# Optimization experiments

Hardware: AMD Instinct MI355X
Metric: run time of the kernel (lower is better)

## Reference

```python
import jax, jax.numpy as jnp
import numpy as np

IN_F, HID, OUT, NN = 64, 128, 64, 128
TOTAL = 4096  # 32 graphs * 128 nodes


def setup_inputs() -> dict:
    key = jax.random.key(0)
    ks = jax.random.split(key, 8)
    d_in = 1 + 2 * IN_F
    s1 = 1.0 / np.sqrt(d_in)
    s2 = 1.0 / np.sqrt(HID)
    return {
        "feat": jax.random.normal(ks[0], (TOTAL, IN_F), jnp.float32),
        "coordinate": jax.random.normal(ks[1], (TOTAL, 3), jnp.float32),
        "W1": jax.random.uniform(ks[2], (d_in, HID), jnp.float32, -s1, s1),
        "b1": jax.random.uniform(ks[3], (HID,), jnp.float32, -s1, s1),
        "W2": jax.random.uniform(ks[4], (HID, HID), jnp.float32, -s2, s2),
        "b2": jax.random.uniform(ks[5], (HID,), jnp.float32, -s2, s2),
        "W3": jax.random.uniform(ks[6], (HID, OUT), jnp.float32, -s2, s2),
        "b3": jax.random.uniform(ks[7], (OUT,), jnp.float32, -s2, s2),
        "num_nodes": NN,
    }


def reference(feat, coordinate, W1, b1, W2, b2, W3, b3, num_nodes):
    N = num_nodes
    B = feat.shape[0] // N
    h = feat.reshape(B, N, -1)        # [B,N,F]
    x = coordinate.reshape(B, N, -1)  # [B,N,3]
    # pairwise squared distance: [B,N,N,1]
    d2 = jnp.sum((x[:, None, :, :] - x[:, :, None, :]) ** 2, axis=-1, keepdims=True)
    F = h.shape[-1]
    # feat concat order matches torch: [h_j broadcast over dim1, h_i broadcast over dim2]
    hj = jnp.broadcast_to(h[:, None, :, :], (B, N, N, F))
    hi = jnp.broadcast_to(h[:, :, None, :], (B, N, N, F))
    z = jnp.concatenate([d2, hj, hi], axis=-1)  # [B,N,N,1+2F]
    z = jax.nn.silu(z @ W1 + b1)
    z = jax.nn.silu(z @ W2 + b2)
    z = z @ W3 + b3                   # [B,N,N,OUT]
    return jnp.sum(z, axis=(1, 2))    # [B,OUT]
```

## Files before the change

### kernel.cpp

```cpp
#include <hip/hip_runtime.h>
#include <hip/hip_bf16.h>

#define F_IN 64
#define HID 128
#define OUTF 64
#define NN 128
#define NB 32
#define TOTAL 4096

typedef short bf16x8 __attribute__((ext_vector_type(8)));
typedef float f32x4 __attribute__((ext_vector_type(4)));

static __device__ __forceinline__ short f2bf(float v) {
  __hip_bfloat16 h = __float2bfloat16(v);
  return __builtin_bit_cast(short, h);
}

static __device__ __forceinline__ float fast_silu(float v) {
  return v * __builtin_amdgcn_rcpf(1.f + __expf(-v));
}

__global__ void prep0(const float* __restrict__ feat,
                      const float* __restrict__ W1,
                      const float* __restrict__ W2,
                      __hip_bfloat16* __restrict__ hb,
                      __hip_bfloat16* __restrict__ wcatT,
                      __hip_bfloat16* __restrict__ w2t) {
  int idx = blockIdx.x * 256 + threadIdx.x;
  if (idx < TOTAL * F_IN) hb[idx] = __float2bfloat16(feat[idx]);
  if (idx < 256 * F_IN) {
    int c = idx >> 6, k = idx & 63;
    float wv = (c < HID) ? W1[(1 + k) * HID + c] : W1[(65 + k) * HID + (c - HID)];
    wcatT[idx] = __float2bfloat16(wv);
  }
  if (idx < HID * HID) {
    int c = idx >> 7, k = idx & 127;
    w2t[c * HID + k] = __float2bfloat16(W2[k * HID + c]);
  }
}

__global__ __launch_bounds__(256) void prep_uv(
    const __hip_bfloat16* __restrict__ hb,
    const __hip_bfloat16* __restrict__ wcatT,
    const float* __restrict__ b1,
    float* __restrict__ uv) {
  const int wave = threadIdx.x >> 6, lane = threadIdx.x & 63;
  const int lr = lane & 15, kg = lane >> 4;
  const int r0 = blockIdx.x * 16;
  f32x4 acc[4];
#pragma unroll
  for (int ct = 0; ct < 4; ++ct) acc[ct] = {0.f, 0.f, 0.f, 0.f};
#pragma unroll
  for (int ks = 0; ks < 2; ++ks) {
    bf16x8 a = *reinterpret_cast<const bf16x8*>(hb + (r0 + lr) * F_IN + ks * 32 + kg * 8);
#pragma unroll
    for (int ct = 0; ct < 4; ++ct) {
      const int c = wave * 64 + ct * 16 + lr;
      bf16x8 w = *reinterpret_cast<const bf16x8*>(
          reinterpret_cast<const short*>(wcatT) + c * F_IN + ks * 32 + kg * 8);
      acc[ct] = __builtin_amdgcn_mfma_f32_16x16x32_bf16(a, w, acc[ct], 0, 0, 0);
    }
  }
#pragma unroll
  for (int ct = 0; ct < 4; ++ct) {
    const int c = wave * 64 + ct * 16 + lr;
    const float badd = (c >= HID) ? b1[c - HID] : 0.f;
#pragma unroll
    for (int reg = 0; reg < 4; ++reg) {
      const int r = r0 + kg * 4 + reg;
      uv[(size_t)r * 256 + c] = acc[ct][reg] + badd;
    }
  }
}

__global__ __launch_bounds__(256) void sake_main(
    const float* __restrict__ coord,
    const float* __restrict__ W1,
    const float* __restrict__ b2,
    const float* __restrict__ uv,
    const __hip_bfloat16* __restrict__ w2t,
    float* __restrict__ part) {
  __shared__ __align__(16) char A1[NN * 256];
  __shared__ float d2s[NN];
  __shared__ float ssum[2][HID];

  const int tid = threadIdx.x;
  const int bid = blockIdx.x;
  const int b = bid >> 7;
  const int i = bid & 127;

  if (tid < NN) {
    const float* xj = coord + (size_t)(b * NN + tid) * 3;
    const float* xi = coord + (size_t)(b * NN + i) * 3;
    float dx = xj[0] - xi[0], dy = xj[1] - xi[1], dz = xj[2] - xi[2];
    d2s[tid] = dx * dx + dy * dy + dz * dz;
  }
  __syncthreads();

  {
    const int cg = tid & 15;
    const int rg = tid >> 4;
    const int c0 = cg * 8;
    const f32x4 w0a = *reinterpret_cast<const f32x4*>(W1 + c0);
    const f32x4 w0b = *reinterpret_cast<const f32x4*>(W1 + c0 + 4);
    const float* vbp = uv + (size_t)(b * NN + i) * 256 + HID + c0;
    const f32x4 vba = *reinterpret_cast<const f32x4*>(vbp);
    const f32x4 vbb = *reinterpret_cast<const f32x4*>(vbp + 4);
#pragma unroll
    for (int it = 0; it < 8; ++it) {
      const int r = rg * 8 + it;
      const float* up = uv + (size_t)(b * NN + r) * 256 + c0;
      const f32x4 ua = *reinterpret_cast<const f32x4*>(up);
      const f32x4 ub = *reinterpret_cast<const f32x4*>(up + 4);
      const float d2r = d2s[r];
      bf16x8 pk;
#pragma unroll
      for (int j = 0; j < 4; ++j)
        pk[j] = f2bf(fast_silu(fmaf(d2r, w0a[j], vba[j] + ua[j])));
#pragma unroll
      for (int j = 0; j < 4; ++j)
        pk[4 + j] = f2bf(fast_silu(fmaf(d2r, w0b[j], vbb[j] + ub[j])));
      const int byo = (cg * 16) ^ (it << 4);
      *reinterpret_cast<bf16x8*>(A1 + r * 256 + byo) = pk;
    }
  }
  __syncthreads();

  const int wave = tid >> 6;
  const int lane = tid & 63;
  const int lr = lane & 15;
  const int kg = lane >> 4;
  const int row_off = (wave >> 1) * 64;
  const int col_off = (wave & 1) * 64;

  f32x4 acc[4][4];
#pragma unroll
  for (int ct = 0; ct < 4; ++ct) {
    const float bb = b2[col_off + ct * 16 + lr];
#pragma unroll
    for (int rt = 0; rt < 4; ++rt)
#pragma unroll
      for (int reg = 0; reg < 4; ++reg) acc[rt][ct][reg] = bb;
  }

#pragma unroll
  for (int ks = 0; ks < 4; ++ks) {
    bf16x8 a[4], w[4];
    const int kb = ks * 64 + kg * 16;
#pragma unroll
    for (int rt = 0; rt < 4; ++rt) {
      const int r = row_off + rt * 16 + lr;
      a[rt] = *reinterpret_cast<const bf16x8*>(A1 + r * 256 + (kb ^ ((r & 7) << 4)));
    }
#pragma unroll
    for (int ct = 0; ct < 4; ++ct) {
      const int c = col_off + ct * 16 + lr;
      w[ct] = *reinterpret_cast<const bf16x8*>(
          reinterpret_cast<const short*>(w2t) + c * HID + ks * 32 + kg * 8);
    }
#pragma unroll
    for (int rt = 0; rt < 4; ++rt)
#pragma unroll
      for (int ct = 0; ct < 4; ++ct)
        acc[rt][ct] = __builtin_amdgcn_mfma_f32_16x16x32_bf16(a[rt], w[ct],
                                                              acc[rt][ct], 0, 0, 0);
  }

  float csum[4];
#pragma unroll
  for (int ct = 0; ct < 4; ++ct) {
    float s = 0.f;
#pragma unroll
    for (int rt = 0; rt < 4; ++rt)
#pragma unroll
      for (int reg = 0; reg < 4; ++reg) s += fast_silu(acc[rt][ct][reg]);
    csum[ct] = s;
  }
#pragma unroll
  for (int ct = 0; ct < 4; ++ct) {
    float s = csum[ct];
    s += __shfl_down(s, 32);
    s += __shfl_down(s, 16);
    csum[ct] = s;
  }
  if (lane < 16) {
    const int sel = wave >> 1;
#pragma unroll
    for (int ct = 0; ct < 4; ++ct)
      ssum[sel][col_off + ct * 16 + lane] = csum[ct];
  }
  __syncthreads();
  if (tid < HID)
    part[(size_t)bid * HID + tid] = ssum[0][tid] + ssum[1][tid];
}

__global__ void final_kernel(const float* __restrict__ part,
                             const float* __restrict__ W3,
                             const float* __restrict__ b3,
                             float* __restrict__ out) {
  __shared__ float s2[2][HID];
  __shared__ float s[HID];
  int b = blockIdx.x, t = threadIdx.x;
  int c = t & 127, half = t >> 7;
  float a = 0.f;
  for (int i = half * 64; i < half * 64 + 64; ++i)
    a += part[(size_t)(b * NN + i) * HID + c];
  s2[half][c] = a;
  __syncthreads();
  if (t < HID) s[t] = s2[0][t] + s2[1][t];
  __syncthreads();
  if (t < OUTF) {
    float o = 16384.f * b3[t];
    for (int c2 = 0; c2 < HID; ++c2) o += s[c2] * W3[c2 * OUTF + t];
    out[b * OUTF + t] = o;
  }
}

extern "C" void kernel_launch(void* const* d_in, const int* in_sizes, int n_in,
                              void* d_out, int out_size, void* d_ws, size_t ws_size,
                              hipStream_t stream) {
  const float* feat = (const float*)d_in[0];
  const float* coord = (const float*)d_in[1];
  const float* W1 = (const float*)d_in[2];
  const float* b1 = (const float*)d_in[3];
  const float* W2 = (const float*)d_in[4];
  const float* b2 = (const float*)d_in[5];
  const float* W3 = (const float*)d_in[6];
  const float* b3 = (const float*)d_in[7];
  float* out = (float*)d_out;

  char* ws = (char*)d_ws;
  __hip_bfloat16* hb = (__hip_bfloat16*)ws;
  __hip_bfloat16* wcatT = (__hip_bfloat16*)(ws + 512 * 1024);
  __hip_bfloat16* w2t = (__hip_bfloat16*)(ws + 544 * 1024);
  float* uv = (float*)(ws + 576 * 1024);
  float* part = (float*)(ws + 576 * 1024 + 4096 * 1024);

  prep0<<<1024, 256, 0, stream>>>(feat, W1, W2, hb, wcatT, w2t);
  prep_uv<<<256, 256, 0, stream>>>(hb, wcatT, b1, uv);
  sake_main<<<TOTAL, 256, 0, stream>>>(coord, W1, b2, uv, w2t, part);
  final_kernel<<<NB, 256, 0, stream>>>(part, W3, b3, out);
}
```

Before: 72.87 us.

## Fuse prep kernels, build first-layer activations in registers, stage W2 in LDS

Merges the two prep kernels into one that converts features and W1 on the fly and writes a swizzled bf16 W2. The main kernel now uses 512 threads, with each wave owning 16 j-rows. It computes the silu layer-1 activations directly into MFMA A-fragments instead of staging them through LDS. It also stages W2 in LDS with an XOR swizzle and remaps block IDs to spread graphs across XCDs. This removes one launch and the A1 LDS round trip, at the cost of every block copying 32KB of W2 from global memory and holding more accumulators per wave.

```diff
diff --git a/kernel.cpp b/kernel.cpp
--- a/kernel.cpp
+++ b/kernel.cpp
@@ -15,49 +15,67 @@
   __hip_bfloat16 h = __float2bfloat16(v);
   return __builtin_bit_cast(short, h);
 }
-
 static __device__ __forceinline__ float fast_silu(float v) {
   return v * __builtin_amdgcn_rcpf(1.f + __expf(-v));
 }
 
-__global__ void prep0(const float* __restrict__ feat,
-                      const float* __restrict__ W1,
-                      const float* __restrict__ W2,
-                      __hip_bfloat16* __restrict__ hb,
-                      __hip_bfloat16* __restrict__ wcatT,
-                      __hip_bfloat16* __restrict__ w2t) {
-  int idx = blockIdx.x * 256 + threadIdx.x;
-  if (idx < TOTAL * F_IN) hb[idx] = __float2bfloat16(feat[idx]);
-  if (idx < 256 * F_IN) {
-    int c = idx >> 6, k = idx & 63;
-    float wv = (c < HID) ? W1[(1 + k) * HID + c] : W1[(65 + k) * HID + (c - HID)];
-    wcatT[idx] = __float2bfloat16(wv);
-  }
-  if (idx < HID * HID) {
-    int c = idx >> 7, k = idx & 127;
-    w2t[c * HID + k] = __float2bfloat16(W2[k * HID + c]);
-  }
-}
-
-__global__ __launch_bounds__(256) void prep_uv(
-    const __hip_bfloat16* __restrict__ hb,
-    const __hip_bfloat16* __restrict__ wcatT,
+__global__ __launch_bounds__(256) void uv_prep(
+    const float* __restrict__ feat,
+    const float* __restrict__ W1,
+    const float* __restrict__ W2,
     const float* __restrict__ b1,
-    float* __restrict__ uv) {
-  const int wave = threadIdx.x >> 6, lane = threadIdx.x & 63;
+    float* __restrict__ uv,
+    __hip_bfloat16* __restrict__ w2swz) {
+  __shared__ __align__(16) char wcat[256 * 128];
+  const int tid = threadIdx.x;
+
+  {
+    const int c = tid;
+    const int cc = c & 127;
+    const int rbase = (c < HID) ? 1 : 65;
+#pragma unroll
+    for (int p = 0; p < 8; ++p) {
+      bf16x8 pk;
+#pragma unroll
+      for (int m = 0; m < 8; ++m)
+        pk[m] = f2bf(W1[(rbase + p * 8 + m) * HID + cc]);
+      *reinterpret_cast<bf16x8*>(wcat + c * 128 + ((p ^ (c & 7)) << 4)) = pk;
+    }
+  }
+  if (blockIdx.x < 64) {
+    const int e = blockIdx.x * 256 + tid;
+    const int kk = e >> 7, cc2 = e & 127;
+    const int byo = cc2 * 256 + (((kk >> 3) ^ (cc2 & 7)) << 4) + (kk & 7) * 2;
+    *reinterpret_cast<__hip_bfloat16*>(reinterpret_cast<char*>(w2swz) + byo) =
+        __float2bfloat16(W2[kk * HID + cc2]);
+  }
+  __syncthreads();
+
+  const int wave = tid >> 6, lane = tid & 63;
   const int lr = lane & 15, kg = lane >> 4;
   const int r0 = blockIdx.x * 16;
+
   f32x4 acc[4];
 #pragma unroll
   for (int ct = 0; ct < 4; ++ct) acc[ct] = {0.f, 0.f, 0.f, 0.f};
+
 #pragma unroll
   for (int ks = 0; ks < 2; ++ks) {
-    bf16x8 a = *reinterpret_cast<const bf16x8*>(hb + (r0 + lr) * F_IN + ks * 32 + kg * 8);
+    const float* fp = feat + (size_t)(r0 + lr) * F_IN + ks * 32 + kg * 8;
+    const f32x4 fa = *reinterpret_cast<const f32x4*>(fp);
+    const f32x4 fb = *reinterpret_cast<const f32x4*>(fp + 4);
+    bf16x8 a;
+#pragma unroll
+    for (int m = 0; m < 4; ++m) {
+      a[m] = f2bf(fa[m]);
+      a[4 + m] = f2bf(fb[m]);
+    }
+    const int slot = ks * 4 + kg;
 #pragma unroll
     for (int ct = 0; ct < 4; ++ct) {
       const int c = wave * 64 + ct * 16 + lr;
-      bf16x8 w = *reinterpret_cast<const bf16x8*>(
-          reinterpret_cast<const short*>(wcatT) + c * F_IN + ks * 32 + kg * 8);
+      const bf16x8 w = *reinterpret_cast<const bf16x8*>(
+          wcat + c * 128 + ((slot ^ (c & 7)) << 4));
       acc[ct] = __builtin_amdgcn_mfma_f32_16x16x32_bf16(a, w, acc[ct], 0, 0, 0);
     }
   }
@@ -73,125 +91,93 @@
   }
 }
 
-__global__ __launch_bounds__(256) void sake_main(
+__global__ __launch_bounds__(512) void sake_main(
     const float* __restrict__ coord,
     const float* __restrict__ W1,
     const float* __restrict__ b2,
     const float* __restrict__ uv,
-    const __hip_bfloat16* __restrict__ w2t,
+    const __hip_bfloat16* __restrict__ w2swz,
     float* __restrict__ part) {
-  __shared__ __align__(16) char A1[NN * 256];
-  __shared__ float d2s[NN];
-  __shared__ float ssum[2][HID];
+  __shared__ __align__(16) char w2lds[HID * 256];
+  __shared__ float ssum[8][HID];
 
   const int tid = threadIdx.x;
-  const int bid = blockIdx.x;
+  const int bid = (blockIdx.x & 7) * 512 + (blockIdx.x >> 3);
   const int b = bid >> 7;
   const int i = bid & 127;
 
-  if (tid < NN) {
-    const float* xj = coord + (size_t)(b * NN + tid) * 3;
-    const float* xi = coord + (size_t)(b * NN + i) * 3;
-    float dx = xj[0] - xi[0], dy = xj[1] - xi[1], dz = xj[2] - xi[2];
-    d2s[tid] = dx * dx + dy * dy + dz * dz;
-  }
-  __syncthreads();
-
-  {
-    const int cg = tid & 15;
-    const int rg = tid >> 4;
-    const int c0 = cg * 8;
-    const f32x4 w0a = *reinterpret_cast<const f32x4*>(W1 + c0);
-    const f32x4 w0b = *reinterpret_cast<const f32x4*>(W1 + c0 + 4);
-    const float* vbp = uv + (size_t)(b * NN + i) * 256 + HID + c0;
-    const f32x4 vba = *reinterpret_cast<const f32x4*>(vbp);
-    const f32x4 vbb = *reinterpret_cast<const f32x4*>(vbp + 4);
-#pragma unroll
-    for (int it = 0; it < 8; ++it) {
-      const int r = rg * 8 + it;
-      const float* up = uv + (size_t)(b * NN + r) * 256 + c0;
-      const f32x4 ua = *reinterpret_cast<const f32x4*>(up);
-      const f32x4 ub = *reinterpret_cast<const f32x4*>(up + 4);
-      const float d2r = d2s[r];
-      bf16x8 pk;
-#pragma unroll
-      for (int j = 0; j < 4; ++j)
-        pk[j] = f2bf(fast_silu(fmaf(d2r, w0a[j], vba[j] + ua[j])));
-#pragma unroll
-      for (int j = 0; j < 4; ++j)
-        pk[4 + j] = f2bf(fast_silu(fmaf(d2r, w0b[j], vbb[j] + ub[j])));
-      const int byo = (cg * 16) ^ (it << 4);
-      *reinterpret_cast<bf16x8*>(A1 + r * 256 + byo) = pk;
-    }
-  }
-  __syncthreads();
-
-  const int wave = tid >> 6;
-  const int lane = tid & 63;
-  const int lr = lane & 15;
-  const int kg = lane >> 4;
-  const int row_off = (wave >> 1) * 64;
-  const int col_off = (wave & 1) * 64;
-
-  f32x4 acc[4][4];
-#pragma unroll
-  for (int ct = 0; ct < 4; ++ct) {
-    const float bb = b2[col_off + ct * 16 + lr];
-#pragma unroll
-    for (int rt = 0; rt < 4; ++rt)
-#pragma unroll
-      for (int reg = 0; reg < 4; ++reg) acc[rt][ct][reg] = bb;
-  }
+#pragma unroll
+  for (int p = 0; p < 4; ++p) {
+    const int o = (tid + p * 512) * 16;
+    *reinterpret_cast<int4*>(w2lds + o) =
+        *reinterpret_cast<const int4*>(reinterpret_cast<const char*>(w2swz) + o);
+  }
+
+  const int wave = tid >> 6, lane = tid & 63;
+  const int lr = lane & 15, kg = lane >> 4;
+  const int j = wave * 16 + lr;
+
+  const float* xj = coord + (size_t)(b * NN + j) * 3;
+  const float* xi = coord + (size_t)(b * NN + i) * 3;
+  const float dx = xj[0] - xi[0], dy = xj[1] - xi[1], dz = xj[2] - xi[2];
+  const float d2j = dx * dx + dy * dy + dz * dz;
+
+  f32x4 acc[8];
+#pragma unroll
+  for (int ct = 0; ct < 8; ++ct) {
+    const float bb = b2[ct * 16 + lr];
+    acc[ct] = {bb, bb, bb, bb};
+  }
+
+  const float* urow = uv + (size_t)(b * NN + j) * 256;
+  const float* vrow = uv + (size_t)(b * NN + i) * 256 + HID;
+
+  __syncthreads();
 
 #pragma unroll
   for (int ks = 0; ks < 4; ++ks) {
-    bf16x8 a[4], w[4];
-    const int kb = ks * 64 + kg * 16;
-#pragma unroll
-    for (int rt = 0; rt < 4; ++rt) {
-      const int r = row_off + rt * 16 + lr;
-      a[rt] = *reinterpret_cast<const bf16x8*>(A1 + r * 256 + (kb ^ ((r & 7) << 4)));
-    }
-#pragma unroll
-    for (int ct = 0; ct < 4; ++ct) {
-      const int c = col_off + ct * 16 + lr;
-      w[ct] = *reinterpret_cast<const bf16x8*>(
-          reinterpret_cast<const short*>(w2t) + c * HID + ks * 32 + kg * 8);
-    }
-#pragma unroll
-    for (int rt = 0; rt < 4; ++rt)
-#pragma unroll
-      for (int ct = 0; ct < 4; ++ct)
-        acc[rt][ct] = __builtin_amdgcn_mfma_f32_16x16x32_bf16(a[rt], w[ct],
-                                                              acc[rt][ct], 0, 0, 0);
-  }
-
-  float csum[4];
-#pragma unroll
-  for (int ct = 0; ct < 4; ++ct) {
+    const int c0 = ks * 32 + kg * 8;
+    const f32x4 ua = *reinterpret_cast<const f32x4*>(urow + c0);
+    const f32x4 ub = *reinterpret_cast<const f32x4*>(urow + c0 + 4);
+    const f32x4 va = *reinterpret_cast<const f32x4*>(vrow + c0);
+    const f32x4 vb = *reinterpret_cast<const f32x4*>(vrow + c0 + 4);
+    const f32x4 wa = *reinterpret_cast<const f32x4*>(W1 + c0);
+    const f32x4 wb = *reinterpret_cast<const f32x4*>(W1 + c0 + 4);
+    bf16x8 a;
+#pragma unroll
+    for (int m = 0; m < 4; ++m) {
+      a[m] = f2bf(fast_silu(fmaf(d2j, wa[m], ua[m] + va[m])));
+      a[4 + m] = f2bf(fast_silu(fmaf(d2j, wb[m], ub[m] + vb[m])));
+    }
+    const int slot = ks * 4 + kg;
+    const int rbase = lr * 256 + ((slot ^ (lr & 7)) << 4);
+#pragma unroll
+    for (int ct = 0; ct < 8; ++ct) {
+      const bf16x8 w = *reinterpret_cast<const bf16x8*>(w2lds + rbase + ct * 4096);
+      acc[ct] = __builtin_amdgcn_mfma_f32_16x16x32_bf16(a, w, acc[ct], 0, 0, 0);
+    }
+  }
+
+  float csum[8];
+#pragma unroll
+  for (int ct = 0; ct < 8; ++ct) {
+    float s = fast_silu(acc[ct][0]) + fast_silu(acc[ct][1]) +
+              fast_silu(acc[ct][2]) + fast_silu(acc[ct][3]);
+    s += __shfl_xor(s, 16);
+    s += __shfl_xor(s, 32);
+    csum[ct] = s;
+  }
+  if (lane < 16) {
+#pragma unroll
+    for (int ct = 0; ct < 8; ++ct) ssum[wave][ct * 16 + lane] = csum[ct];
+  }
+  __syncthreads();
+  if (tid < HID) {
     float s = 0.f;
 #pragma unroll
-    for (int rt = 0; rt < 4; ++rt)
-#pragma unroll
-      for (int reg = 0; reg < 4; ++reg) s += fast_silu(acc[rt][ct][reg]);
-    csum[ct] = s;
-  }
-#pragma unroll
-  for (int ct = 0; ct < 4; ++ct) {
-    float s = csum[ct];
-    s += __shfl_down(s, 32);
-    s += __shfl_down(s, 16);
-    csum[ct] = s;
-  }
-  if (lane < 16) {
-    const int sel = wave >> 1;
-#pragma unroll
-    for (int ct = 0; ct < 4; ++ct)
-      ssum[sel][col_off + ct * 16 + lane] = csum[ct];
-  }
-  __syncthreads();
-  if (tid < HID)
-    part[(size_t)bid * HID + tid] = ssum[0][tid] + ssum[1][tid];
+    for (int w = 0; w < 8; ++w) s += ssum[w][tid];
+    part[(size_t)bid * HID + tid] = s;
+  }
 }
 
 __global__ void final_kernel(const float* __restrict__ part,
@@ -230,14 +216,11 @@
   float* out = (float*)d_out;
 
   char* ws = (char*)d_ws;
-  __hip_bfloat16* hb = (__hip_bfloat16*)ws;
-  __hip_bfloat16* wcatT = (__hip_bfloat16*)(ws + 512 * 1024);
-  __hip_bfloat16* w2t = (__hip_bfloat16*)(ws + 544 * 1024);
-  float* uv = (float*)(ws + 576 * 1024);
-  float* part = (float*)(ws + 576 * 1024 + 4096 * 1024);
-
-  prep0<<<1024, 256, 0, stream>>>(feat, W1, W2, hb, wcatT, w2t);
-  prep_uv<<<256, 256, 0, stream>>>(hb, wcatT, b1, uv);
-  sake_main<<<TOTAL, 256, 0, stream>>>(coord, W1, b2, uv, w2t, part);
+  __hip_bfloat16* w2swz = (__hip_bfloat16*)ws;
+  float* uv = (float*)(ws + 64 * 1024);
+  float* part = (float*)(ws + 64 * 1024 + 4096 * 1024);
+
+  uv_prep<<<256, 256, 0, stream>>>(feat, W1, W2, b1, uv, w2swz);
+  sake_main<<<TOTAL, 512, 0, stream>>>(coord, W1, b2, uv, w2swz, part);
   final_kernel<<<NB, 256, 0, stream>>>(part, W3, b3, out);
 }
```

Result: faster. 70.54 us (-3.2%).
